# Kernel tuning notes

Hardware: AMD Instinct MI355X
Metric: run time of the kernel (lower is better)

The kernel has to match this reference:

```python
import jax, jax.numpy as jnp
import numpy as np

B, S, D, H, FF = 4, 2048, 1024, 16, 4096
HD = D // H
EPS = 1e-5


def layer_norm(x, g, b):
    mu = jnp.mean(x, axis=-1, keepdims=True)
    var = jnp.mean(jnp.square(x - mu), axis=-1, keepdims=True)
    return (x - mu) * jax.lax.rsqrt(var + EPS) * g + b


def setup_inputs() -> dict:
    key = jax.random.key(0)
    ks = jax.random.split(key, 8)
    s_d = 1.0 / np.sqrt(D)
    s_ff = 1.0 / np.sqrt(FF)
    return {
        "x": jax.random.normal(ks[0], (B, S, D), dtype=jnp.float32),
        "Wq": jax.random.normal(ks[1], (D, D), dtype=jnp.float32) * s_d,
        "bq": jnp.zeros((D,), jnp.float32),
        "Wk": jax.random.normal(ks[2], (D, D), dtype=jnp.float32) * s_d,
        "bk": jnp.zeros((D,), jnp.float32),
        "Wv": jax.random.normal(ks[3], (D, D), dtype=jnp.float32) * s_d,
        "bv": jnp.zeros((D,), jnp.float32),
        "g1": jnp.ones((D,), jnp.float32),
        "beta1": jnp.zeros((D,), jnp.float32),
        "g2": jnp.ones((D,), jnp.float32),
        "beta2": jnp.zeros((D,), jnp.float32),
        "W1": jax.random.normal(ks[4], (D, FF), dtype=jnp.float32) * s_d,
        "b1": jnp.zeros((FF,), jnp.float32),
        "W2": jax.random.normal(ks[5], (FF, D), dtype=jnp.float32) * s_ff,
        "b2": jnp.zeros((D,), jnp.float32),
    }


def reference(x, Wq, bq, Wk, bk, Wv, bv, g1, beta1, g2, beta2, W1, b1, W2, b2):
    # pre-LN attention (self.layer_norm in the original)
    h = layer_norm(x, g1, beta1)
    q = (h @ Wq + bq).reshape(B, S, H, HD)
    k = (h @ Wk + bk).reshape(B, S, H, HD)
    v = (h @ Wv + bv).reshape(B, S, H, HD)
    scores = jnp.einsum("bqhd,bkhd->bhqk", q, k) / np.sqrt(HD)
    probs = jax.nn.softmax(scores, axis=-1)
    attn = jnp.einsum("bhqk,bkhd->bqhd", probs, v).reshape(B, S, D)
    y = attn + x
    # second LN (self.LN), then FFN; note original adds residual from LN output
    f = layer_norm(y, g2, beta2)
    ff = jnp.maximum(f @ W1 + b1, 0.0) @ W2 + b2
    return f + ff
```

## Files before the change

### kernel.cpp

```cpp
#include <hip/hip_runtime.h>
#include <hip/hip_bf16.h>
#include <cstdint>
#include <cstddef>

#define B_   4
#define S_   2048
#define D_   1024
#define H_   16
#define HD_  64
#define FF_  4096
#define MTOT (B_*S_)

typedef __bf16 bf16;
typedef bf16  bf16x8 __attribute__((ext_vector_type(8)));
typedef bf16  bf16x4 __attribute__((ext_vector_type(4)));
typedef float f32x4  __attribute__((ext_vector_type(4)));

#define LOG2E 1.44269504088896340736f

__device__ __forceinline__ void async16(const bf16* g, bf16* l) {
  __builtin_amdgcn_global_load_lds(
      (const __attribute__((address_space(1))) unsigned int*)g,
      (__attribute__((address_space(3))) unsigned int*)l,
      16, 0, 0);
}

__global__ void wcast_t(const float* __restrict__ W, bf16* __restrict__ Wt,
                        int K, int N) {
  __shared__ float t[32][33];
  const int k0 = blockIdx.y * 32, n0 = blockIdx.x * 32;
  const int tx = threadIdx.x, ty = threadIdx.y;
#pragma unroll
  for (int r = ty; r < 32; r += 8)
    t[r][tx] = W[(size_t)(k0 + r) * N + n0 + tx];
  __syncthreads();
#pragma unroll
  for (int r = ty; r < 32; r += 8)
    Wt[(size_t)(n0 + r) * K + k0 + tx] = (bf16)t[tx][r];
}

__global__ void ln_fused(const float* __restrict__ xin, const float* __restrict__ res,
                         const float* __restrict__ gamma, const float* __restrict__ beta,
                         bf16* __restrict__ out) {
  const int row = blockIdx.x, tid = threadIdx.x;
  const int lane = tid & 63, w = tid >> 6;
  f32x4 v = *(const f32x4*)(xin + (size_t)row * D_ + tid * 4);
  if (res) {
    f32x4 r = *(const f32x4*)(res + (size_t)row * D_ + tid * 4);
    v += r;
  }
  float sum = v[0] + v[1] + v[2] + v[3];
  float sq  = v[0]*v[0] + v[1]*v[1] + v[2]*v[2] + v[3]*v[3];
#pragma unroll
  for (int d = 1; d < 64; d <<= 1) {
    sum += __shfl_xor(sum, d);
    sq  += __shfl_xor(sq, d);
  }
  __shared__ float red[8];
  if (lane == 0) { red[w] = sum; red[4 + w] = sq; }
  __syncthreads();
  sum = red[0] + red[1] + red[2] + red[3];
  sq  = red[4] + red[5] + red[6] + red[7];
  const float mu   = sum * (1.f / D_);
  const float rstd = rsqrtf(sq * (1.f / D_) - mu * mu + 1e-5f);
  f32x4 g  = *(const f32x4*)(gamma + tid * 4);
  f32x4 bt = *(const f32x4*)(beta  + tid * 4);
  bf16x4 ov;
#pragma unroll
  for (int j = 0; j < 4; j++)
    ov[j] = (bf16)((v[j] - mu) * rstd * g[j] + bt[j]);
  *(bf16x4*)(out + (size_t)row * D_ + tid * 4) = ov;
}

template <int EPI>
__global__ void gemm_bt(const bf16* __restrict__ A, const bf16* __restrict__ Bt,
                        const float* __restrict__ bias, void* __restrict__ Cout,
                        const bf16* __restrict__ addf, int M, int N, int K) {
  __shared__ bf16 As[128 * 32];
  __shared__ bf16 Bs[128 * 32];
  const int tid = threadIdx.x;
  const int lane = tid & 63;
  const int w = tid >> 6;
  const int wm = w >> 1, wn = w & 1;
  const int bm = blockIdx.y * 128;
  const int bn = blockIdx.x * 128;
  const int rg = lane >> 4, rl = lane & 15;

  const bf16* ga = A  + (size_t)(bm + w * 16 + (lane >> 2)) * K + (lane & 3) * 8;
  const bf16* gb = Bt + (size_t)(bn + w * 16 + (lane >> 2)) * K + (lane & 3) * 8;
  bf16* la = As + w * 512;
  bf16* lb = Bs + w * 512;
  const size_t rowadv = (size_t)64 * K;

  f32x4 acc[4][4];
  const f32x4 z = {0.f, 0.f, 0.f, 0.f};
#pragma unroll
  for (int m = 0; m < 4; m++)
#pragma unroll
    for (int n = 0; n < 4; n++) acc[m][n] = z;

  for (int kt = 0; kt < K; kt += 32) {
    __syncthreads();
    async16(ga,          la);
    async16(ga + rowadv, la + 2048);
    async16(gb,          lb);
    async16(gb + rowadv, lb + 2048);
    ga += 32; gb += 32;
    __syncthreads();

    bf16x8 af[4], bfr[4];
#pragma unroll
    for (int m = 0; m < 4; m++)
      af[m] = *(const bf16x8*)(As + (wm * 64 + m * 16 + rl) * 32 + rg * 8);
#pragma unroll
    for (int n = 0; n < 4; n++)
      bfr[n] = *(const bf16x8*)(Bs + (wn * 64 + n * 16 + rl) * 32 + rg * 8);
#pragma unroll
    for (int m = 0; m < 4; m++)
#pragma unroll
      for (int n = 0; n < 4; n++)
        acc[m][n] = __builtin_amdgcn_mfma_f32_16x16x32_bf16(af[m], bfr[n], acc[m][n], 0, 0, 0);
  }

#pragma unroll
  for (int m = 0; m < 4; m++) {
    const int row0 = bm + wm * 64 + m * 16 + rg * 4;
#pragma unroll
    for (int n = 0; n < 4; n++) {
      const int col = bn + wn * 64 + n * 16 + rl;
      const float bb = bias[col];
#pragma unroll
      for (int i = 0; i < 4; i++) {
        const int row = row0 + i;
        float v = acc[m][n][i] + bb;
        if (EPI == 3) {
          ((bf16*)Cout)[(size_t)row * N + col] = (bf16)fmaxf(v, 0.f);
        } else {
          ((float*)Cout)[(size_t)row * N + col] =
              v + (float)addf[(size_t)row * N + col];
        }
      }
    }
  }
}

__global__ void gemm_qkv(const bf16* __restrict__ A, const bf16* __restrict__ Bt,
                         const float* __restrict__ bq, const float* __restrict__ bk,
                         const float* __restrict__ bv, bf16* __restrict__ qout,
                         bf16* __restrict__ kout, bf16* __restrict__ vtout) {
  const int K = 1024;
  __shared__ bf16 As[128 * 32];
  __shared__ bf16 Bs[128 * 32];
  const int tid = threadIdx.x;
  const int lane = tid & 63;
  const int w = tid >> 6;
  const int wm = w >> 1, wn = w & 1;
  const int bm = blockIdx.y * 128;
  const int bn = blockIdx.x * 128;
  const int rg = lane >> 4, rl = lane & 15;

  const bf16* ga = A  + (size_t)(bm + w * 16 + (lane >> 2)) * K + (lane & 3) * 8;
  const bf16* gb = Bt + (size_t)(bn + w * 16 + (lane >> 2)) * K + (lane & 3) * 8;
  bf16* la = As + w * 512;
  bf16* lb = Bs + w * 512;
  const size_t rowadv = (size_t)64 * K;

  f32x4 acc[4][4];
  const f32x4 z = {0.f, 0.f, 0.f, 0.f};
#pragma unroll
  for (int m = 0; m < 4; m++)
#pragma unroll
    for (int n = 0; n < 4; n++) acc[m][n] = z;

  for (int kt = 0; kt < K; kt += 32) {
    __syncthreads();
    async16(ga,          la);
    async16(ga + rowadv, la + 2048);
    async16(gb,          lb);
    async16(gb + rowadv, lb + 2048);
    ga += 32; gb += 32;
    __syncthreads();

    bf16x8 af[4], bfr[4];
#pragma unroll
    for (int m = 0; m < 4; m++)
      af[m] = *(const bf16x8*)(As + (wm * 64 + m * 16 + rl) * 32 + rg * 8);
#pragma unroll
    for (int n = 0; n < 4; n++)
      bfr[n] = *(const bf16x8*)(Bs + (wn * 64 + n * 16 + rl) * 32 + rg * 8);
#pragma unroll
    for (int m = 0; m < 4; m++)
#pragma unroll
      for (int n = 0; n < 4; n++)
        acc[m][n] = __builtin_amdgcn_mfma_f32_16x16x32_bf16(af[m], bfr[n], acc[m][n], 0, 0, 0);
  }

  const int sector = bn >> 10;
#pragma unroll
  for (int m = 0; m < 4; m++) {
    const int row0 = bm + wm * 64 + m * 16 + rg * 4;
#pragma unroll
    for (int n = 0; n < 4; n++) {
      const int col = bn + wn * 64 + n * 16 + rl;
      const int cl = col & 1023;
      const float bb = (sector == 0) ? bq[cl] : (sector == 1 ? bk[cl] : bv[cl]);
#pragma unroll
      for (int i = 0; i < 4; i++) {
        const int row = row0 + i;
        const float v = acc[m][n][i] + bb;
        if (sector == 0) {
          qout[(size_t)row * D_ + cl] = (bf16)(v * (0.125f * LOG2E));
        } else if (sector == 1) {
          kout[(size_t)row * D_ + cl] = (bf16)v;
        } else {
          const int b = row >> 11, s = row & 2047;
          const int h = cl >> 6, hd = cl & 63;
          vtout[(((size_t)(b * H_ + h) * HD_ + hd) << 11) + s] = (bf16)v;
        }
      }
    }
  }
}

__global__ __launch_bounds__(256, 4)
void attn_fwd(const bf16* __restrict__ Q, const bf16* __restrict__ Kb,
              const bf16* __restrict__ Vt, float* __restrict__ O) {
  __shared__ bf16 Pl[4][32][72];
  const int tid = threadIdx.x, lane = tid & 63, w = tid >> 6;
  const int rg = lane >> 4, rl = lane & 15;
  const int bh = blockIdx.y, b = bh >> 4, h = bh & 15;
  const int q0 = blockIdx.x * 128 + w * 32;

  const bf16* qp = Q + ((size_t)b * S_ + q0) * D_ + h * HD_;
  const bf16* kp = Kb + (size_t)b * S_ * D_ + h * HD_;
  const bf16* vp = Vt + (size_t)bh * HD_ * S_;

  bf16x8 qf[2][2];
#pragma unroll
  for (int m = 0; m < 2; m++)
#pragma unroll
    for (int kc = 0; kc < 2; kc++)
      qf[m][kc] = *(const bf16x8*)(qp + (size_t)(m * 16 + rl) * D_ + kc * 32 + rg * 8);

  const f32x4 z = {0.f, 0.f, 0.f, 0.f};
  f32x4 o[2][4];
  float mr[2], lr[2];
#pragma unroll
  for (int m = 0; m < 2; m++) {
    mr[m] = -1e30f; lr[m] = 0.f;
#pragma unroll
    for (int np = 0; np < 4; np++) o[m][np] = z;
  }

  for (int t = 0; t < S_ / 64; ++t) {
    const bf16* kt = kp + (size_t)t * 64 * D_;
    bf16x8 kf[4][2];
#pragma unroll
    for (int n = 0; n < 4; n++)
#pragma unroll
      for (int kc = 0; kc < 2; kc++)
        kf[n][kc] = *(const bf16x8*)(kt + (size_t)(n * 16 + rl) * D_ + kc * 32 + rg * 8);

    f32x4 s[2][4];
#pragma unroll
    for (int m = 0; m < 2; m++)
#pragma unroll
      for (int n = 0; n < 4; n++) s[m][n] = z;
#pragma unroll
    for (int kc = 0; kc < 2; kc++)
#pragma unroll
      for (int n = 0; n < 4; n++)
#pragma unroll
        for (int m = 0; m < 2; m++)
          s[m][n] = __builtin_amdgcn_mfma_f32_16x16x32_bf16(kf[n][kc], qf[m][kc], s[m][n], 0, 0, 0);

    bf16x8 vf[4][2];
#pragma unroll
    for (int np = 0; np < 4; np++)
#pragma unroll
      for (int kc = 0; kc < 2; kc++)
        vf[np][kc] = *(const bf16x8*)(vp + (size_t)(np * 16 + rl) * S_ + t * 64 + kc * 32 + rg * 8);

#pragma unroll
    for (int m = 0; m < 2; m++) {
      float x0 = fmaxf(fmaxf(s[m][0][0], s[m][0][1]), fmaxf(s[m][0][2], s[m][0][3]));
      float x1 = fmaxf(fmaxf(s[m][1][0], s[m][1][1]), fmaxf(s[m][1][2], s[m][1][3]));
      float x2 = fmaxf(fmaxf(s[m][2][0], s[m][2][1]), fmaxf(s[m][2][2], s[m][2][3]));
      float x3 = fmaxf(fmaxf(s[m][3][0], s[m][3][1]), fmaxf(s[m][3][2], s[m][3][3]));
      float vmax = fmaxf(fmaxf(x0, x1), fmaxf(x2, x3));
      vmax = fmaxf(vmax, __shfl_xor(vmax, 16));
      vmax = fmaxf(vmax, __shfl_xor(vmax, 32));
      const float mnew = fmaxf(mr[m], vmax);
      const float corr = __builtin_amdgcn_exp2f(mr[m] - mnew);
      mr[m] = mnew;
      float ps = 0.f;
#pragma unroll
      for (int n = 0; n < 4; n++)
#pragma unroll
        for (int i = 0; i < 4; i++) {
          const float p = __builtin_amdgcn_exp2f(s[m][n][i] - mnew);
          s[m][n][i] = p;
          ps += p;
        }
      ps += __shfl_xor(ps, 16);
      ps += __shfl_xor(ps, 32);
      lr[m] = lr[m] * corr + ps;
#pragma unroll
      for (int np = 0; np < 4; np++)
#pragma unroll
        for (int i = 0; i < 4; i++) o[m][np][i] *= corr;
#pragma unroll
      for (int n = 0; n < 4; n++) {
        bf16x4 pv;
#pragma unroll
        for (int i = 0; i < 4; i++) pv[i] = (bf16)s[m][n][i];
        *(bf16x4*)&Pl[w][m * 16 + rl][n * 16 + rg * 4] = pv;
      }
    }

    bf16x8 pf[2][2];
#pragma unroll
    for (int m = 0; m < 2; m++)
#pragma unroll
      for (int kc = 0; kc < 2; kc++)
        pf[m][kc] = *(const bf16x8*)&Pl[w][m * 16 + rl][kc * 32 + rg * 8];

#pragma unroll
    for (int kc = 0; kc < 2; kc++)
#pragma unroll
      for (int np = 0; np < 4; np++)
#pragma unroll
        for (int m = 0; m < 2; m++)
          o[m][np] = __builtin_amdgcn_mfma_f32_16x16x32_bf16(vf[np][kc], pf[m][kc], o[m][np], 0, 0, 0);
  }

#pragma unroll
  for (int m = 0; m < 2; m++) {
    const float inv = 1.f / lr[m];
    const size_t rowb = ((size_t)b * S_ + q0 + m * 16 + rl) * D_ + h * HD_;
#pragma unroll
    for (int np = 0; np < 4; np++) {
      f32x4 ov;
#pragma unroll
      for (int i = 0; i < 4; i++) ov[i] = o[m][np][i] * inv;
      *(f32x4*)(O + rowb + np * 16 + rg * 4) = ov;
    }
  }
}

extern "C" void kernel_launch(void* const* d_in, const int* in_sizes, int n_in,
                              void* d_out, int out_size, void* d_ws, size_t ws_size,
                              hipStream_t stream) {
  (void)in_sizes; (void)n_in; (void)out_size; (void)ws_size;
  const float* x   = (const float*)d_in[0];
  const float* Wq  = (const float*)d_in[1];
  const float* bq  = (const float*)d_in[2];
  const float* Wk  = (const float*)d_in[3];
  const float* bk  = (const float*)d_in[4];
  const float* Wv  = (const float*)d_in[5];
  const float* bv  = (const float*)d_in[6];
  const float* g1  = (const float*)d_in[7];
  const float* be1 = (const float*)d_in[8];
  const float* g2  = (const float*)d_in[9];
  const float* be2 = (const float*)d_in[10];
  const float* W1  = (const float*)d_in[11];
  const float* b1  = (const float*)d_in[12];
  const float* W2  = (const float*)d_in[13];
  const float* b2  = (const float*)d_in[14];
  float* out = (float*)d_out;

  char* p = (char*)d_ws;
  const size_t MB = (size_t)1 << 20;
  bf16*  wqkv = (bf16*)(p + 0 * MB);
  bf16*  w1t  = (bf16*)(p + 6 * MB);
  bf16*  w2t  = (bf16*)(p + 14 * MB);
  bf16*  hb   = (bf16*)(p + 22 * MB);
  bf16*  qb   = (bf16*)(p + 38 * MB);
  bf16*  kb   = (bf16*)(p + 54 * MB);
  bf16*  vt   = (bf16*)(p + 70 * MB);
  float* at   = (float*)(p + 86 * MB);
  bf16*  fb   = (bf16*)(p + 118 * MB);
  bf16*  ff1  = (bf16*)(p + 22 * MB);

  const dim3 tb(32, 8);
  wcast_t<<<dim3(32, 32),  tb, 0, stream>>>(Wq, wqkv,                1024, 1024);
  wcast_t<<<dim3(32, 32),  tb, 0, stream>>>(Wk, wqkv + 1024 * 1024,  1024, 1024);
  wcast_t<<<dim3(32, 32),  tb, 0, stream>>>(Wv, wqkv + 2048 * 1024,  1024, 1024);
  wcast_t<<<dim3(128, 32), tb, 0, stream>>>(W1, w1t, 1024, 4096);
  wcast_t<<<dim3(32, 128), tb, 0, stream>>>(W2, w2t, 4096, 1024);

  ln_fused<<<MTOT, 256, 0, stream>>>(x, nullptr, g1, be1, hb);

  gemm_qkv<<<dim3(24, 64), 256, 0, stream>>>(hb, wqkv, bq, bk, bv, qb, kb, vt);

  attn_fwd<<<dim3(16, 64), 256, 0, stream>>>(qb, kb, vt, at);

  ln_fused<<<MTOT, 256, 0, stream>>>(at, x, g2, be2, fb);

  gemm_bt<3><<<dim3(32, 64), 256, 0, stream>>>(fb, w1t, b1, ff1, nullptr, MTOT, 4096, 1024);
  gemm_bt<4><<<dim3(8, 64),  256, 0, stream>>>(ff1, w2t, b2, out, fb, MTOT, 1024, 4096);
}
```

Before: 663.7 us.

## Stage K/V tiles in double-buffered swizzled LDS shared by 8-wave attention blocks

The attention kernel now uses 512-thread blocks covering 256 queries. Each wave asynchronously loads part of the next 64-key K and V tile into double-buffered, XOR-swizzled shared memory. Previously every wave read K and V straight from global memory, so the idea is to share those tiles across 8 waves and overlap their loading with compute. The cost is a block-wide barrier every iteration, more LDS per block, and half as many blocks in the grid.

```diff
diff --git a/kernel.cpp b/kernel.cpp
--- a/kernel.cpp
+++ b/kernel.cpp
@@ -222,19 +222,31 @@
   }
 }
 
-__global__ __launch_bounds__(256, 4)
+__global__ __launch_bounds__(512, 4)
 void attn_fwd(const bf16* __restrict__ Q, const bf16* __restrict__ Kb,
               const bf16* __restrict__ Vt, float* __restrict__ O) {
-  __shared__ bf16 Pl[4][32][72];
+  __shared__ bf16 Ks[2][64 * 64];
+  __shared__ bf16 Vs[2][64 * 64];
+  __shared__ bf16 Pl[8][32][72];
   const int tid = threadIdx.x, lane = tid & 63, w = tid >> 6;
   const int rg = lane >> 4, rl = lane & 15;
   const int bh = blockIdx.y, b = bh >> 4, h = bh & 15;
-  const int q0 = blockIdx.x * 128 + w * 32;
+  const int q0 = blockIdx.x * 256 + w * 32;
 
   const bf16* qp = Q + ((size_t)b * S_ + q0) * D_ + h * HD_;
   const bf16* kp = Kb + (size_t)b * S_ * D_ + h * HD_;
   const bf16* vp = Vt + (size_t)bh * HD_ * S_;
 
+  const int sr = lane >> 3;
+  const int sc = (lane & 7) ^ sr;
+
+#define STAGE(buf, t)                                                          \
+  {                                                                            \
+    const int row = w * 8 + sr;                                                \
+    async16(kp + (size_t)((t) * 64 + row) * D_ + sc * 8, &Ks[buf][w * 8 * 64]);\
+    async16(vp + (size_t)row * S_ + (t) * 64 + sc * 8,  &Vs[buf][w * 8 * 64]); \
+  }
+
   bf16x8 qf[2][2];
 #pragma unroll
   for (int m = 0; m < 2; m++)
@@ -252,14 +264,23 @@
     for (int np = 0; np < 4; np++) o[m][np] = z;
   }
 
+  STAGE(0, 0);
+  __syncthreads();
+
+  int cur = 0;
   for (int t = 0; t < S_ / 64; ++t) {
-    const bf16* kt = kp + (size_t)t * 64 * D_;
+    if (t + 1 < S_ / 64) STAGE(cur ^ 1, t + 1);
+    const bf16* Kc = Ks[cur];
+    const bf16* Vc = Vs[cur];
+
     bf16x8 kf[4][2];
 #pragma unroll
-    for (int n = 0; n < 4; n++)
+    for (int n = 0; n < 4; n++) {
+      const int krow = n * 16 + rl;
 #pragma unroll
       for (int kc = 0; kc < 2; kc++)
-        kf[n][kc] = *(const bf16x8*)(kt + (size_t)(n * 16 + rl) * D_ + kc * 32 + rg * 8);
+        kf[n][kc] = *(const bf16x8*)(Kc + krow * 64 + (((kc * 4 + rg) ^ (krow & 7)) * 8));
+    }
 
     f32x4 s[2][4];
 #pragma unroll
@@ -273,13 +294,6 @@
 #pragma unroll
         for (int m = 0; m < 2; m++)
           s[m][n] = __builtin_amdgcn_mfma_f32_16x16x32_bf16(kf[n][kc], qf[m][kc], s[m][n], 0, 0, 0);
-
-    bf16x8 vf[4][2];
-#pragma unroll
-    for (int np = 0; np < 4; np++)
-#pragma unroll
-      for (int kc = 0; kc < 2; kc++)
-        vf[np][kc] = *(const bf16x8*)(vp + (size_t)(np * 16 + rl) * S_ + t * 64 + kc * 32 + rg * 8);
 
 #pragma unroll
     for (int m = 0; m < 2; m++) {
@@ -325,6 +339,15 @@
       for (int kc = 0; kc < 2; kc++)
         pf[m][kc] = *(const bf16x8*)&Pl[w][m * 16 + rl][kc * 32 + rg * 8];
 
+    bf16x8 vf[4][2];
+#pragma unroll
+    for (int np = 0; np < 4; np++) {
+      const int vrow = np * 16 + rl;
+#pragma unroll
+      for (int kc = 0; kc < 2; kc++)
+        vf[np][kc] = *(const bf16x8*)(Vc + vrow * 64 + (((kc * 4 + rg) ^ (vrow & 7)) * 8));
+    }
+
 #pragma unroll
     for (int kc = 0; kc < 2; kc++)
 #pragma unroll
@@ -332,7 +355,11 @@
 #pragma unroll
         for (int m = 0; m < 2; m++)
           o[m][np] = __builtin_amdgcn_mfma_f32_16x16x32_bf16(vf[np][kc], pf[m][kc], o[m][np], 0, 0, 0);
-  }
+
+    __syncthreads();
+    cur ^= 1;
+  }
+#undef STAGE
 
 #pragma unroll
   for (int m = 0; m < 2; m++) {
@@ -393,7 +420,7 @@
 
   gemm_qkv<<<dim3(24, 64), 256, 0, stream>>>(hb, wqkv, bq, bk, bv, qb, kb, vt);
 
-  attn_fwd<<<dim3(16, 64), 256, 0, stream>>>(qb, kb, vt, at);
+  attn_fwd<<<dim3(8, 64), 512, 0, stream>>>(qb, kb, vt, at);
 
   ln_fused<<<MTOT, 256, 0, stream>>>(at, x, g2, be2, fb);
 
```

Measured after the change: 544.8 us. -17.9%, faster.
